# Optimization experiments

Hardware: AMD Instinct MI355X
Metric: run time of the kernel (lower is better)

## Reference

```python
import math
import jax, jax.numpy as jnp
import numpy as np

B, V, N, D = 256, 16, 1024, 512
CLIP = 10.0


def setup_inputs() -> dict:
    key = jax.random.key(0)
    ks = jax.random.split(key, 9)
    s = 0.02
    return {
        "g_node": jax.random.normal(ks[0], (B, D), jnp.float32),
        "Z_veh": jax.random.normal(ks[1], (B, V, D), jnp.float32),
        "g_graph": jax.random.normal(ks[2], (B, D), jnp.float32),
        "Z_node": jax.random.normal(ks[3], (B, N, D), jnp.float32),
        "mask": jax.random.randint(ks[4], (B, N), 0, 2).astype(bool),
        "W_ctx": jax.random.normal(ks[5], (D, 3 * D), jnp.float32) * s,
        "b_ctx": jnp.zeros((D,), jnp.float32),
        "Wq": jax.random.normal(ks[6], (D, D), jnp.float32) * s,
        "Wk": jax.random.normal(ks[7], (D, D), jnp.float32) * s,
    }


def reference(g_node, Z_veh, g_graph, Z_node, mask, W_ctx, b_ctx, Wq, Wk):
    scale = math.sqrt(Z_node.shape[-1])
    # concat -> Linear(3D, D) -> ReLU   (torch Linear: x @ W.T + b)
    cat = jnp.concatenate([g_node, Z_veh.mean(axis=1), g_graph], axis=-1)  # [B,3D]
    ctx = jax.nn.relu(cat @ W_ctx.T + b_ctx)  # [B,D]
    Q = ctx @ Wq.T  # [B,D]
    K = jnp.einsum("bnd,ed->bne", Z_node, Wk)  # [B,N,D]
    logits = jnp.einsum("bd,bnd->bn", Q, K) / scale  # [B,N]
    logits = CLIP * jnp.tanh(logits)
    logits = jnp.where(mask, logits, -jnp.inf)
    return logits
```

## Files before the change

### kernel.cpp

```cpp
#include <hip/hip_runtime.h>
#include <math.h>

#define Bz  256
#define Vz  16
#define Nz  1024
#define Dz  512
#define TD  1536
#define INV_SCALE 0.04419417382415922f
#define MASKED_VAL -1.0e30f


__global__ __launch_bounds__(256) void k0_zm(const float* __restrict__ Z_veh,
                                             float* __restrict__ Zm)
{
    const int idx = blockIdx.x * 256 + threadIdx.x;
    const int b   = idx >> 7;
    const int d4  = (idx & 127) * 4;
    const float* p = Z_veh + (size_t)b * Vz * Dz + d4;
    float4 s = {0.f, 0.f, 0.f, 0.f};
#pragma unroll
    for (int v = 0; v < Vz; ++v) {
        float4 t = *(const float4*)(p + (size_t)v * Dz);
        s.x += t.x; s.y += t.y; s.z += t.z; s.w += t.w;
    }
    s.x *= 0.0625f; s.y *= 0.0625f; s.z *= 0.0625f; s.w *= 0.0625f;
    *(float4*)&Zm[(size_t)b * Dz + d4] = s;
}

__global__ __launch_bounds__(256) void kA(const float* __restrict__ g_node,
                                          const float* __restrict__ Zm,
                                          const float* __restrict__ g_graph,
                                          const float* __restrict__ W_ctx,
                                          const float* __restrict__ Wq,
                                          const float* __restrict__ Wk,
                                          float* __restrict__ Cp2,
                                          float* __restrict__ GP)
{
    __shared__ float As[16][64];
    __shared__ float Bs[16][64];
    const int tid = threadIdx.x;
    const int tm = tid >> 4;
    const int tn = tid & 15;
    float acc[4][4] = {};

    if (blockIdx.x < 256) {
        const int idx = blockIdx.x;
        const int m0 = (idx >> 5) * 64;
        const int n0 = ((idx >> 3) & 3) * 64;
        const int kz = idx & 7;
        const int ar = tid >> 2, ac = (tid & 3) * 4;
        const int br = tid >> 2, bc = (tid & 3) * 4;

        float4 va, vb;
        {
            const int k0   = kz * 192;
            const int reg  = k0 >> 9;
            const int kloc = k0 & 511;
            va = *(const float4*)&W_ctx[(size_t)(m0 + ar) * TD + k0 + ac];
            const float* bsrc = (reg == 0) ? g_node : (reg == 2) ? g_graph : Zm;
            vb = *(const float4*)&bsrc[(size_t)(n0 + br) * Dz + kloc + bc];
        }

        for (int kt = 0; kt < 192; kt += 16) {
            __syncthreads();
            As[ac + 0][ar] = va.x; As[ac + 1][ar] = va.y;
            As[ac + 2][ar] = va.z; As[ac + 3][ar] = va.w;
            Bs[bc + 0][br] = vb.x; Bs[bc + 1][br] = vb.y;
            Bs[bc + 2][br] = vb.z; Bs[bc + 3][br] = vb.w;
            __syncthreads();
            if (kt + 16 < 192) {
                const int k0   = kz * 192 + kt + 16;
                const int reg  = k0 >> 9;
                const int kloc = k0 & 511;
                va = *(const float4*)&W_ctx[(size_t)(m0 + ar) * TD + k0 + ac];
                const float* bsrc = (reg == 0) ? g_node : (reg == 2) ? g_graph : Zm;
                vb = *(const float4*)&bsrc[(size_t)(n0 + br) * Dz + kloc + bc];
            }
#pragma unroll
            for (int kk = 0; kk < 16; ++kk) {
                float4 a  = *(const float4*)&As[kk][tm * 4];
                float4 bb = *(const float4*)&Bs[kk][tn * 4];
                float av[4] = {a.x, a.y, a.z, a.w};
                float bv[4] = {bb.x, bb.y, bb.z, bb.w};
#pragma unroll
                for (int i = 0; i < 4; ++i)
#pragma unroll
                    for (int j = 0; j < 4; ++j)
                        acc[i][j] += av[i] * bv[j];
            }
        }
#pragma unroll
        for (int i = 0; i < 4; ++i) {
            float4 v = {acc[i][0], acc[i][1], acc[i][2], acc[i][3]};
            *(float4*)&Cp2[((size_t)kz * Dz + m0 + tm * 4 + i) * Bz + n0 + tn * 4] = v;
        }
    } else {
        const int g  = blockIdx.x - 256;
        const int m0 = (g >> 5) * 64;
        const int n0 = ((g >> 2) & 7) * 64;
        const int kz = g & 3;
        const int r = tid >> 4, c = (tid & 15) * 4;

        float4 va = *(const float4*)&Wq[(size_t)(kz * 128 + r) * Dz + m0 + c];
        float4 vb = *(const float4*)&Wk[(size_t)(kz * 128 + r) * Dz + n0 + c];

        for (int kt = 0; kt < 128; kt += 16) {
            __syncthreads();
            *(float4*)&As[r][c] = va;
            *(float4*)&Bs[r][c] = vb;
            __syncthreads();
            if (kt + 16 < 128) {
                const int k0 = kz * 128 + kt + 16;
                va = *(const float4*)&Wq[(size_t)(k0 + r) * Dz + m0 + c];
                vb = *(const float4*)&Wk[(size_t)(k0 + r) * Dz + n0 + c];
            }
#pragma unroll
            for (int kk = 0; kk < 16; ++kk) {
                float4 a  = *(const float4*)&As[kk][tm * 4];
                float4 bb = *(const float4*)&Bs[kk][tn * 4];
                float av[4] = {a.x, a.y, a.z, a.w};
                float bv[4] = {bb.x, bb.y, bb.z, bb.w};
#pragma unroll
                for (int i = 0; i < 4; ++i)
#pragma unroll
                    for (int j = 0; j < 4; ++j)
                        acc[i][j] += av[i] * bv[j];
            }
        }
#pragma unroll
        for (int i = 0; i < 4; ++i) {
            float4 v = {acc[i][0], acc[i][1], acc[i][2], acc[i][3]};
            *(float4*)&GP[((size_t)kz * Dz + m0 + tm * 4 + i) * Dz + n0 + tn * 4] = v;
        }
    }
}

__global__ __launch_bounds__(256) void kB(const float* __restrict__ Cp2,
                                          const float* __restrict__ bias,
                                          const float* __restrict__ GP,
                                          float* __restrict__ QkP)
{
    __shared__ float As[16][64];
    __shared__ float Bs[16][64];
    const int m0 = blockIdx.x * 64;
    const int n0 = blockIdx.y * 64;
    const int kz = blockIdx.z;
    const int tid = threadIdx.x;
    const int tm = tid >> 4, tn = tid & 15;
    const int r = tid >> 4, col = (tid & 15) * 4;

    float4 cp[8], gp[4];
    float bv;
    {
        const int k0 = kz * 64;
#pragma unroll
        for (int z = 0; z < 8; ++z)
            cp[z] = *(const float4*)&Cp2[((size_t)z * Dz + k0 + r) * Bz + m0 + col];
#pragma unroll
        for (int z = 0; z < 4; ++z)
            gp[z] = *(const float4*)&GP[((size_t)z * Dz + k0 + r) * Dz + n0 + col];
        bv = bias[k0 + r];
    }

    float acc[4][4] = {};
    for (int kt = 0; kt < 64; kt += 16) {
        float4 s = {0.f, 0.f, 0.f, 0.f};
#pragma unroll
        for (int z = 0; z < 8; ++z) {
            s.x += cp[z].x; s.y += cp[z].y; s.z += cp[z].z; s.w += cp[z].w;
        }
        s.x = fmaxf(s.x + bv, 0.f); s.y = fmaxf(s.y + bv, 0.f);
        s.z = fmaxf(s.z + bv, 0.f); s.w = fmaxf(s.w + bv, 0.f);
        float4 t = {0.f, 0.f, 0.f, 0.f};
#pragma unroll
        for (int z = 0; z < 4; ++z) {
            t.x += gp[z].x; t.y += gp[z].y; t.z += gp[z].z; t.w += gp[z].w;
        }
        __syncthreads();
        *(float4*)&As[r][col] = s;
        *(float4*)&Bs[r][col] = t;
        __syncthreads();
        if (kt + 16 < 64) {
            const int k0 = kz * 64 + kt + 16;
#pragma unroll
            for (int z = 0; z < 8; ++z)
                cp[z] = *(const float4*)&Cp2[((size_t)z * Dz + k0 + r) * Bz + m0 + col];
#pragma unroll
            for (int z = 0; z < 4; ++z)
                gp[z] = *(const float4*)&GP[((size_t)z * Dz + k0 + r) * Dz + n0 + col];
            bv = bias[k0 + r];
        }
#pragma unroll
        for (int kk = 0; kk < 16; ++kk) {
            float4 a  = *(const float4*)&As[kk][tm * 4];
            float4 bb = *(const float4*)&Bs[kk][tn * 4];
            float av[4] = {a.x, a.y, a.z, a.w};
            float bv2[4] = {bb.x, bb.y, bb.z, bb.w};
#pragma unroll
            for (int i = 0; i < 4; ++i)
#pragma unroll
                for (int j = 0; j < 4; ++j)
                    acc[i][j] += av[i] * bv2[j];
        }
    }
#pragma unroll
    for (int i = 0; i < 4; ++i) {
        float4 v = {acc[i][0], acc[i][1], acc[i][2], acc[i][3]};
        *(float4*)&QkP[((size_t)kz * Bz + m0 + tm * 4 + i) * Dz + n0 + tn * 4] = v;
    }
}

__global__ __launch_bounds__(256) void kC(const float* __restrict__ Z,
                                          const float* __restrict__ QkP,
                                          const unsigned char* __restrict__ mask,
                                          float* __restrict__ out)
{
    __shared__ float q_sh[Dz];
    const int b    = blockIdx.y;
    const int n0   = blockIdx.x * 64;
    const int tid  = threadIdx.x;

    {
        const int c2 = tid * 2;
        float2 s = {0.f, 0.f};
#pragma unroll
        for (int z = 0; z < 8; ++z) {
            float2 p = *(const float2*)&QkP[((size_t)z * Bz + b) * Dz + c2];
            s.x += p.x; s.y += p.y;
        }
        *(float2*)&q_sh[c2] = s;
    }
    __syncthreads();

    const int lane = tid & 63;
    const int wave = tid >> 6;
    const int grp  = lane >> 4;
    const int gl   = lane & 15;

    float4 q[8];
#pragma unroll
    for (int j = 0; j < 8; ++j)
        q[j] = *(const float4*)&q_sh[j * 64 + gl * 4];

    const float* zb = Z + ((size_t)b * Nz + n0) * Dz;

#pragma unroll
    for (int it = 0; it < 4; ++it) {
        const int r = wave * 16 + it * 4 + grp;
        const float* zp = zb + (size_t)r * Dz + gl * 4;
        float acc = 0.f;
#pragma unroll
        for (int j = 0; j < 8; ++j) {
            float4 z4 = *(const float4*)(zp + j * 64);
            acc += q[j].x * z4.x + q[j].y * z4.y + q[j].z * z4.z + q[j].w * z4.w;
        }
        acc += __shfl_xor(acc, 1, 64);
        acc += __shfl_xor(acc, 2, 64);
        acc += __shfl_xor(acc, 4, 64);
        acc += __shfl_xor(acc, 8, 64);
        if (gl == 0) {
            const int nn = n0 + r;
            float v = 10.0f * tanhf(acc * INV_SCALE);
            out[(size_t)b * Nz + nn] =
                mask[(size_t)b * Nz + nn] ? v : MASKED_VAL;
        }
    }
}

extern "C" void kernel_launch(void* const* d_in, const int* in_sizes, int n_in,
                              void* d_out, int out_size, void* d_ws, size_t ws_size,
                              hipStream_t stream)
{
    const float* g_node  = (const float*)d_in[0];
    const float* Z_veh   = (const float*)d_in[1];
    const float* g_graph = (const float*)d_in[2];
    const float* Z_node  = (const float*)d_in[3];
    const unsigned char* mask = (const unsigned char*)d_in[4];
    const float* W_ctx   = (const float*)d_in[5];
    const float* b_ctx   = (const float*)d_in[6];
    const float* Wq      = (const float*)d_in[7];
    const float* Wk      = (const float*)d_in[8];
    float* out = (float*)d_out;

    float* ws  = (float*)d_ws;
    float* Zm  = ws;
    float* Cp2 = ws + 131072;
    float* GP  = ws + 1179648;
    float* QkP = ws + 2228224;

    k0_zm<<<dim3(128), 256, 0, stream>>>(Z_veh, Zm);

    kA<<<dim3(512), 256, 0, stream>>>(g_node, Zm, g_graph, W_ctx, Wq, Wk,
                                      Cp2, GP);

    kB<<<dim3(4, 8, 8), 256, 0, stream>>>(Cp2, b_ctx, GP, QkP);

    kC<<<dim3(Nz / 64, Bz), 256, 0, stream>>>(Z_node, QkP, mask, out);
}
```

Measured before the change: 132.1 us.

## Double-buffer shared tiles in GEMM kernels and use nontemporal vector loads in kC

Converts the three small GEMM kernels (kA both branches, kB) to double-buffered shared memory, so each k-step needs one barrier instead of two and the next tile is written while the current one is read. In kC, the Z_node stream is read with nontemporal loads and accumulated with a 4-wide vector FMA before the horizontal sum. The aim is lower barrier overhead in the GEMMs and less cache pollution in the dominant bandwidth-bound dot-product kernel. Shared memory per block doubles, and the kC summation order changes slightly.

```diff
diff --git a/kernel.cpp b/kernel.cpp
--- a/kernel.cpp
+++ b/kernel.cpp
@@ -9,6 +9,8 @@
 #define INV_SCALE 0.04419417382415922f
 #define MASKED_VAL -1.0e30f
 
+
+typedef float f4 __attribute__((ext_vector_type(4)));
 
 __global__ __launch_bounds__(256) void k0_zm(const float* __restrict__ Z_veh,
                                              float* __restrict__ Zm)
@@ -36,8 +38,8 @@
                                           float* __restrict__ Cp2,
                                           float* __restrict__ GP)
 {
-    __shared__ float As[16][64];
-    __shared__ float Bs[16][64];
+    __shared__ float As[2][16][64];
+    __shared__ float Bs[2][16][64];
     const int tid = threadIdx.x;
     const int tm = tid >> 4;
     const int tn = tid & 15;
@@ -51,24 +53,25 @@
         const int ar = tid >> 2, ac = (tid & 3) * 4;
         const int br = tid >> 2, bc = (tid & 3) * 4;
 
-        float4 va, vb;
         {
             const int k0   = kz * 192;
             const int reg  = k0 >> 9;
             const int kloc = k0 & 511;
-            va = *(const float4*)&W_ctx[(size_t)(m0 + ar) * TD + k0 + ac];
+            float4 va = *(const float4*)&W_ctx[(size_t)(m0 + ar) * TD + k0 + ac];
             const float* bsrc = (reg == 0) ? g_node : (reg == 2) ? g_graph : Zm;
-            vb = *(const float4*)&bsrc[(size_t)(n0 + br) * Dz + kloc + bc];
-        }
-
+            float4 vb = *(const float4*)&bsrc[(size_t)(n0 + br) * Dz + kloc + bc];
+            As[0][ac + 0][ar] = va.x; As[0][ac + 1][ar] = va.y;
+            As[0][ac + 2][ar] = va.z; As[0][ac + 3][ar] = va.w;
+            Bs[0][bc + 0][br] = vb.x; Bs[0][bc + 1][br] = vb.y;
+            Bs[0][bc + 2][br] = vb.z; Bs[0][bc + 3][br] = vb.w;
+        }
+
+        int cur = 0;
         for (int kt = 0; kt < 192; kt += 16) {
             __syncthreads();
-            As[ac + 0][ar] = va.x; As[ac + 1][ar] = va.y;
-            As[ac + 2][ar] = va.z; As[ac + 3][ar] = va.w;
-            Bs[bc + 0][br] = vb.x; Bs[bc + 1][br] = vb.y;
-            Bs[bc + 2][br] = vb.z; Bs[bc + 3][br] = vb.w;
-            __syncthreads();
-            if (kt + 16 < 192) {
+            float4 va, vb;
+            const bool more = (kt + 16 < 192);
+            if (more) {
                 const int k0   = kz * 192 + kt + 16;
                 const int reg  = k0 >> 9;
                 const int kloc = k0 & 511;
@@ -78,8 +81,8 @@
             }
 #pragma unroll
             for (int kk = 0; kk < 16; ++kk) {
-                float4 a  = *(const float4*)&As[kk][tm * 4];
-                float4 bb = *(const float4*)&Bs[kk][tn * 4];
+                float4 a  = *(const float4*)&As[cur][kk][tm * 4];
+                float4 bb = *(const float4*)&Bs[cur][kk][tn * 4];
                 float av[4] = {a.x, a.y, a.z, a.w};
                 float bv[4] = {bb.x, bb.y, bb.z, bb.w};
 #pragma unroll
@@ -87,6 +90,14 @@
 #pragma unroll
                     for (int j = 0; j < 4; ++j)
                         acc[i][j] += av[i] * bv[j];
+            }
+            if (more) {
+                const int nxt = cur ^ 1;
+                As[nxt][ac + 0][ar] = va.x; As[nxt][ac + 1][ar] = va.y;
+                As[nxt][ac + 2][ar] = va.z; As[nxt][ac + 3][ar] = va.w;
+                Bs[nxt][bc + 0][br] = vb.x; Bs[nxt][bc + 1][br] = vb.y;
+                Bs[nxt][bc + 2][br] = vb.z; Bs[nxt][bc + 3][br] = vb.w;
+                cur = nxt;
             }
         }
 #pragma unroll
@@ -101,23 +112,27 @@
         const int kz = g & 3;
         const int r = tid >> 4, c = (tid & 15) * 4;
 
-        float4 va = *(const float4*)&Wq[(size_t)(kz * 128 + r) * Dz + m0 + c];
-        float4 vb = *(const float4*)&Wk[(size_t)(kz * 128 + r) * Dz + n0 + c];
-
+        {
+            float4 va = *(const float4*)&Wq[(size_t)(kz * 128 + r) * Dz + m0 + c];
+            float4 vb = *(const float4*)&Wk[(size_t)(kz * 128 + r) * Dz + n0 + c];
+            *(float4*)&As[0][r][c] = va;
+            *(float4*)&Bs[0][r][c] = vb;
+        }
+
+        int cur = 0;
         for (int kt = 0; kt < 128; kt += 16) {
             __syncthreads();
-            *(float4*)&As[r][c] = va;
-            *(float4*)&Bs[r][c] = vb;
-            __syncthreads();
-            if (kt + 16 < 128) {
+            float4 va, vb;
+            const bool more = (kt + 16 < 128);
+            if (more) {
                 const int k0 = kz * 128 + kt + 16;
                 va = *(const float4*)&Wq[(size_t)(k0 + r) * Dz + m0 + c];
                 vb = *(const float4*)&Wk[(size_t)(k0 + r) * Dz + n0 + c];
             }
 #pragma unroll
             for (int kk = 0; kk < 16; ++kk) {
-                float4 a  = *(const float4*)&As[kk][tm * 4];
-                float4 bb = *(const float4*)&Bs[kk][tn * 4];
+                float4 a  = *(const float4*)&As[cur][kk][tm * 4];
+                float4 bb = *(const float4*)&Bs[cur][kk][tn * 4];
                 float av[4] = {a.x, a.y, a.z, a.w};
                 float bv[4] = {bb.x, bb.y, bb.z, bb.w};
 #pragma unroll
@@ -125,6 +140,12 @@
 #pragma unroll
                     for (int j = 0; j < 4; ++j)
                         acc[i][j] += av[i] * bv[j];
+            }
+            if (more) {
+                const int nxt = cur ^ 1;
+                *(float4*)&As[nxt][r][c] = va;
+                *(float4*)&Bs[nxt][r][c] = vb;
+                cur = nxt;
             }
         }
 #pragma unroll
@@ -140,8 +161,8 @@
                                           const float* __restrict__ GP,
                                           float* __restrict__ QkP)
 {
-    __shared__ float As[16][64];
-    __shared__ float Bs[16][64];
+    __shared__ float As[2][16][64];
+    __shared__ float Bs[2][16][64];
     const int m0 = blockIdx.x * 64;
     const int n0 = blockIdx.y * 64;
     const int kz = blockIdx.z;
@@ -149,6 +170,23 @@
     const int tm = tid >> 4, tn = tid & 15;
     const int r = tid >> 4, col = (tid & 15) * 4;
 
+    auto fold_write = [&](int buf, const float4* cp, const float4* gp, float bv) {
+        float4 s = {0.f, 0.f, 0.f, 0.f};
+#pragma unroll
+        for (int z = 0; z < 8; ++z) {
+            s.x += cp[z].x; s.y += cp[z].y; s.z += cp[z].z; s.w += cp[z].w;
+        }
+        s.x = fmaxf(s.x + bv, 0.f); s.y = fmaxf(s.y + bv, 0.f);
+        s.z = fmaxf(s.z + bv, 0.f); s.w = fmaxf(s.w + bv, 0.f);
+        float4 t = {0.f, 0.f, 0.f, 0.f};
+#pragma unroll
+        for (int z = 0; z < 4; ++z) {
+            t.x += gp[z].x; t.y += gp[z].y; t.z += gp[z].z; t.w += gp[z].w;
+        }
+        *(float4*)&As[buf][r][col] = s;
+        *(float4*)&Bs[buf][r][col] = t;
+    };
+
     float4 cp[8], gp[4];
     float bv;
     {
@@ -160,27 +198,15 @@
         for (int z = 0; z < 4; ++z)
             gp[z] = *(const float4*)&GP[((size_t)z * Dz + k0 + r) * Dz + n0 + col];
         bv = bias[k0 + r];
+        fold_write(0, cp, gp, bv);
     }
 
     float acc[4][4] = {};
+    int cur = 0;
     for (int kt = 0; kt < 64; kt += 16) {
-        float4 s = {0.f, 0.f, 0.f, 0.f};
-#pragma unroll
-        for (int z = 0; z < 8; ++z) {
-            s.x += cp[z].x; s.y += cp[z].y; s.z += cp[z].z; s.w += cp[z].w;
-        }
-        s.x = fmaxf(s.x + bv, 0.f); s.y = fmaxf(s.y + bv, 0.f);
-        s.z = fmaxf(s.z + bv, 0.f); s.w = fmaxf(s.w + bv, 0.f);
-        float4 t = {0.f, 0.f, 0.f, 0.f};
-#pragma unroll
-        for (int z = 0; z < 4; ++z) {
-            t.x += gp[z].x; t.y += gp[z].y; t.z += gp[z].z; t.w += gp[z].w;
-        }
         __syncthreads();
-        *(float4*)&As[r][col] = s;
-        *(float4*)&Bs[r][col] = t;
-        __syncthreads();
-        if (kt + 16 < 64) {
+        const bool more = (kt + 16 < 64);
+        if (more) {
             const int k0 = kz * 64 + kt + 16;
 #pragma unroll
             for (int z = 0; z < 8; ++z)
@@ -192,8 +218,8 @@
         }
 #pragma unroll
         for (int kk = 0; kk < 16; ++kk) {
-            float4 a  = *(const float4*)&As[kk][tm * 4];
-            float4 bb = *(const float4*)&Bs[kk][tn * 4];
+            float4 a  = *(const float4*)&As[cur][kk][tm * 4];
+            float4 bb = *(const float4*)&Bs[cur][kk][tn * 4];
             float av[4] = {a.x, a.y, a.z, a.w};
             float bv2[4] = {bb.x, bb.y, bb.z, bb.w};
 #pragma unroll
@@ -201,6 +227,10 @@
 #pragma unroll
                 for (int j = 0; j < 4; ++j)
                     acc[i][j] += av[i] * bv2[j];
+        }
+        if (more) {
+            fold_write(cur ^ 1, cp, gp, bv);
+            cur ^= 1;
         }
     }
 #pragma unroll
@@ -237,10 +267,10 @@
     const int grp  = lane >> 4;
     const int gl   = lane & 15;
 
-    float4 q[8];
+    f4 q[8];
 #pragma unroll
     for (int j = 0; j < 8; ++j)
-        q[j] = *(const float4*)&q_sh[j * 64 + gl * 4];
+        q[j] = *(const f4*)&q_sh[j * 64 + gl * 4];
 
     const float* zb = Z + ((size_t)b * Nz + n0) * Dz;
 
@@ -248,12 +278,13 @@
     for (int it = 0; it < 4; ++it) {
         const int r = wave * 16 + it * 4 + grp;
         const float* zp = zb + (size_t)r * Dz + gl * 4;
-        float acc = 0.f;
+        f4 a4 = {0.f, 0.f, 0.f, 0.f};
 #pragma unroll
         for (int j = 0; j < 8; ++j) {
-            float4 z4 = *(const float4*)(zp + j * 64);
-            acc += q[j].x * z4.x + q[j].y * z4.y + q[j].z * z4.z + q[j].w * z4.w;
-        }
+            f4 z4 = __builtin_nontemporal_load((const f4*)(zp + j * 64));
+            a4 += q[j] * z4;
+        }
+        float acc = (a4.x + a4.y) + (a4.z + a4.w);
         acc += __shfl_xor(acc, 1, 64);
         acc += __shfl_xor(acc, 2, 64);
         acc += __shfl_xor(acc, 4, 64);
```

Result: faster. 120.1 us (median of 2 runs) (-9.1%).
